# Kernel optimization log

Measured on AMD Instinct MI355X. Metric: run time of the kernel, lower is better.

## Reference

```python
import jax, jax.numpy as jnp
import numpy as np

N, E, L, S = 20000, 100000, 128, 6   # nodes, edges, latent, message-passing steps
NF, EF, TW, OUT = 11, 5, 5, 1        # node feat, edge feat, time_window, output_size
LN_EPS = 1e-5


def _mlp_ln(x, W1, b1, W2, b2, g, beta):
    # Linear -> ReLU -> Linear -> ReLU -> LayerNorm (matches torch Sequential)
    h = jax.nn.relu(x @ W1 + b1)
    h = jax.nn.relu(h @ W2 + b2)
    mu = h.mean(-1, keepdims=True)
    var = ((h - mu) ** 2).mean(-1, keepdims=True)
    return (h - mu) * jax.lax.rsqrt(var + LN_EPS) * g + beta


def setup_inputs() -> dict:
    key = jax.random.key(0)
    ks = iter(jax.random.split(key, 64))

    def w(shape):
        fan_in = shape[-2]
        return jax.random.normal(next(ks), shape, jnp.float32) / np.float32(np.sqrt(fan_in))

    inp = {
        'node_features': jax.random.normal(next(ks), (1, N, NF), jnp.float32),
        'edge_features': jax.random.normal(next(ks), (1, E, EF), jnp.float32),
        'senders': jax.random.randint(next(ks), (E,), 0, N, jnp.int32),
        'receivers': jax.random.randint(next(ks), (E,), 0, N, jnp.int32),
        'node_mean': jax.random.normal(next(ks), (NF,), jnp.float32),
        'node_std': jnp.ones((NF,), jnp.float32),
        'edge_mean': jax.random.normal(next(ks), (EF,), jnp.float32),
        'edge_std': jnp.ones((EF,), jnp.float32),
        'enc_n_W1': w((NF, L)), 'enc_n_b1': jnp.zeros((L,), jnp.float32),
        'enc_n_W2': w((L, L)), 'enc_n_b2': jnp.zeros((L,), jnp.float32),
        'enc_n_g': jnp.ones((L,), jnp.float32), 'enc_n_beta': jnp.zeros((L,), jnp.float32),
        'enc_e_W1': w((EF, L)), 'enc_e_b1': jnp.zeros((L,), jnp.float32),
        'enc_e_W2': w((L, L)), 'enc_e_b2': jnp.zeros((L,), jnp.float32),
        'enc_e_g': jnp.ones((L,), jnp.float32), 'enc_e_beta': jnp.zeros((L,), jnp.float32),
        'blk_e_W1': w((S, 3 * L, L)), 'blk_e_b1': jnp.zeros((S, L), jnp.float32),
        'blk_e_W2': w((S, L, L)), 'blk_e_b2': jnp.zeros((S, L), jnp.float32),
        'blk_e_g': jnp.ones((S, L), jnp.float32), 'blk_e_beta': jnp.zeros((S, L), jnp.float32),
        'blk_n_W1': w((S, 2 * L, L)), 'blk_n_b1': jnp.zeros((S, L), jnp.float32),
        'blk_n_W2': w((S, L, L)), 'blk_n_b2': jnp.zeros((S, L), jnp.float32),
        'blk_n_g': jnp.ones((S, L), jnp.float32), 'blk_n_beta': jnp.zeros((S, L), jnp.float32),
        'dec_W1': w((L, 8)), 'dec_b1': jnp.zeros((8,), jnp.float32),
        'dec_W2': w((8, TW)), 'dec_b2': jnp.zeros((TW,), jnp.float32),
    }
    return inp


def reference(node_features, edge_features, senders, receivers,
              node_mean, node_std, edge_mean, edge_std,
              enc_n_W1, enc_n_b1, enc_n_W2, enc_n_b2, enc_n_g, enc_n_beta,
              enc_e_W1, enc_e_b1, enc_e_W2, enc_e_b2, enc_e_g, enc_e_beta,
              blk_e_W1, blk_e_b1, blk_e_W2, blk_e_b2, blk_e_g, blk_e_beta,
              blk_n_W1, blk_n_b1, blk_n_W2, blk_n_b2, blk_n_g, blk_n_beta,
              dec_W1, dec_b1, dec_W2, dec_b2):
    # ---- encode (Normalizer in eval mode: (x - mean) / std) ----
    node_lat = _mlp_ln((node_features - node_mean) / node_std,
                       enc_n_W1, enc_n_b1, enc_n_W2, enc_n_b2, enc_n_g, enc_n_beta)  # [1,N,L]
    edge_lat = _mlp_ln((edge_features - edge_mean) / edge_std,
                       enc_e_W1, enc_e_b1, enc_e_W2, enc_e_b2, enc_e_g, enc_e_beta)  # [1,E,L]

    # ---- process: gather -> edge MLP -> scatter_add -> node MLP, residuals ----
    for i in range(S):
        e_in = jnp.concatenate([node_lat[:, senders, :], node_lat[:, receivers, :], edge_lat], axis=-1)  # [1,E,3L]
        new_e = _mlp_ln(e_in, blk_e_W1[i], blk_e_b1[i], blk_e_W2[i], blk_e_b2[i], blk_e_g[i], blk_e_beta[i])
        aggr = jax.ops.segment_sum(new_e[0], receivers, num_segments=N)[None]  # [1,N,L]
        new_n = _mlp_ln(jnp.concatenate([node_lat, aggr], axis=-1),
                        blk_n_W1[i], blk_n_b1[i], blk_n_W2[i], blk_n_b2[i], blk_n_g[i], blk_n_beta[i])
        node_lat = node_lat + new_n
        edge_lat = edge_lat + new_e

    # ---- decode: Conv1d(k=1) == per-node linear; Swish(beta=1) ----
    h = node_lat[0] @ dec_W1 + dec_b1          # [N,8]
    h = h * jax.nn.sigmoid(h)
    dec = h @ dec_W2 + dec_b2                  # [N,TW]
    dt = jnp.repeat(jnp.arange(1, TW + 1), OUT).astype(dec.dtype)  # [TW*OUT]
    delta = (dec * dt).reshape(N, TW, OUT).transpose(1, 0, 2)      # [TW,N,OUT]
    return delta
```

## Files before the change

### kernel.cpp

```cpp
#include <hip/hip_runtime.h>
#include <cstdint>
#include <cstddef>


#define N_NODES 20000
#define N_EDGES 100000
#define LDIM    128
#define NSTEPS  6

typedef float  f32x4  __attribute__((ext_vector_type(4)));
typedef __bf16 bf16x8 __attribute__((ext_vector_type(8)));

__device__ __forceinline__ bf16x8 cvt8(const float* p) {
  float4 u = *(const float4*)p;
  float4 v = *(const float4*)(p + 4);
  bf16x8 o;
  o[0] = (__bf16)u.x; o[1] = (__bf16)u.y; o[2] = (__bf16)u.z; o[3] = (__bf16)u.w;
  o[4] = (__bf16)v.x; o[5] = (__bf16)v.y; o[6] = (__bf16)v.z; o[7] = (__bf16)v.w;
  return o;
}

struct PrepArgs {
  const float *s_enW1, *s_enW2, *s_eeW1, *s_eeW2;
  const float *s_beW1, *s_beW2, *s_bnW1, *s_bnW2;
  __bf16 *d_enW1, *d_enW2, *d_eeW1, *d_eeW2;
  __bf16 *d_beW1, *d_beW2, *d_bnW1, *d_bnW2;
  int* counts;
};

__device__ __forceinline__ void swz_src(int idx, int& k, int& col) {
  int j    = idx & 7;
  int lane = (idx >> 3) & 63;
  int ct   = (idx >> 9) & 7;
  int kc   = idx >> 12;
  col = ct * 16 + (lane & 15);
  k   = kc * 32 + (lane >> 4) * 8 + j;
}

__global__ __launch_bounds__(256) void prep_kernel(PrepArgs p) {
  int idx = blockIdx.x * 256 + threadIdx.x;
  int k, col;

  if (idx < 4096) {
    swz_src(idx, k, col);
    p.d_enW1[idx] = (__bf16)((k < 11) ? p.s_enW1[k * 128 + col] : 0.f);
    return;
  }
  idx -= 4096;
  if (idx < 16384) {
    swz_src(idx, k, col);
    p.d_enW2[idx] = (__bf16)p.s_enW2[k * 128 + col];
    return;
  }
  idx -= 16384;
  if (idx < 4096) {
    swz_src(idx, k, col);
    p.d_eeW1[idx] = (__bf16)((k < 5) ? p.s_eeW1[k * 128 + col] : 0.f);
    return;
  }
  idx -= 4096;
  if (idx < 16384) {
    swz_src(idx, k, col);
    p.d_eeW2[idx] = (__bf16)p.s_eeW2[k * 128 + col];
    return;
  }
  idx -= 16384;
  if (idx < 294912) {
    int s = idx / 49152, rem = idx % 49152;
    swz_src(rem, k, col);
    p.d_beW1[idx] = (__bf16)p.s_beW1[(size_t)s * 49152 + k * 128 + col];
    return;
  }
  idx -= 294912;
  if (idx < 98304) {
    int s = idx >> 14, rem = idx & 16383;
    swz_src(rem, k, col);
    p.d_beW2[idx] = (__bf16)p.s_beW2[s * 16384 + k * 128 + col];
    return;
  }
  idx -= 98304;
  if (idx < 196608) {
    int s = idx >> 15, rem = idx & 32767;
    swz_src(rem, k, col);
    p.d_bnW1[idx] = (__bf16)p.s_bnW1[s * 32768 + k * 128 + col];
    return;
  }
  idx -= 196608;
  if (idx < 98304) {
    int s = idx >> 14, rem = idx & 16383;
    swz_src(rem, k, col);
    p.d_bnW2[idx] = (__bf16)p.s_bnW2[s * 16384 + k * 128 + col];
    return;
  }
  idx -= 98304;
  if (idx < N_NODES) p.counts[idx] = 0;
}

__global__ __launch_bounds__(256) void hist_kernel(const int* __restrict__ recv,
                                                   int* __restrict__ counts) {
  int e = blockIdx.x * 256 + threadIdx.x;
  if (e < N_EDGES) atomicAdd(&counts[recv[e]], 1);
}

__global__ __launch_bounds__(1024) void scan_kernel(const int* __restrict__ counts,
                                                    int* __restrict__ row_ptr,
                                                    int* __restrict__ cursor) {
  __shared__ int part[1024];
  const int t = threadIdx.x;
  const int base = t * 20;
  int local[20];
  int s = 0;
#pragma unroll
  for (int i = 0; i < 20; ++i) {
    int idx = base + i;
    int v = (idx < N_NODES) ? counts[idx] : 0;
    local[i] = s;
    s += v;
  }
  part[t] = s;
  __syncthreads();
  for (int off = 1; off < 1024; off <<= 1) {
    int add = (t >= off) ? part[t - off] : 0;
    __syncthreads();
    part[t] += add;
    __syncthreads();
  }
  const int excl = part[t] - s;
#pragma unroll
  for (int i = 0; i < 20; ++i) {
    int idx = base + i;
    if (idx < N_NODES) {
      int v = excl + local[i];
      row_ptr[idx] = v;
      cursor[idx]  = v;
    }
  }
  if (t == 1023) row_ptr[N_NODES] = part[1023];
}

__global__ __launch_bounds__(256) void fill_kernel(const int* __restrict__ recv,
                                                   int* __restrict__ cursor,
                                                   int* __restrict__ edge_list) {
  int e = blockIdx.x * 256 + threadIdx.x;
  if (e < N_EDGES) {
    int r = recv[e];
    int pos = atomicAdd(&cursor[r], 1);
    edge_list[pos] = e;
  }
}

struct MlpArgs {
  const float* x; const float* mean; const float* stdv;
  float* node_lat; float* edge_lat;
  __bf16* new_e;
  const int* senders; const int* receivers;
  const int* row_ptr; const int* edge_list;
  const __bf16* W1t; const __bf16* W2t;
  const float* b1; const float* b2; const float* g; const float* beta;
  int M;
};

template <int K1, int MODE>
__global__ __launch_bounds__(256, 3) void mlp2_kernel(MlpArgs a) {
  constexpr int NKC = K1 / 32;
  constexpr int RT  = 2;
  constexpr int HS  = 136;

  __shared__ __align__(16) __bf16 H1[4 * 32 * HS];

  const int tid   = threadIdx.x;
  const int lane  = tid & 63;
  const int wv    = tid >> 6;
  const int l15   = lane & 15;
  const int quad  = lane >> 4;
  const int M     = a.M;
  const int rbase = blockIdx.x * 128 + wv * 32;

  __bf16* h1w = H1 + wv * 32 * HS;

  int rowA[RT];
#pragma unroll
  for (int rt = 0; rt < RT; ++rt) {
    int r = rbase + rt * 16 + l15;
    rowA[rt] = (r < M) ? r : (M - 1);
  }

  int sA[RT], rA[RT];
  if constexpr (MODE == 2) {
#pragma unroll
    for (int rt = 0; rt < RT; ++rt) {
      sA[rt] = a.senders[rowA[rt]];
      rA[rt] = a.receivers[rowA[rt]];
    }
  }

  if constexpr (MODE == 3) {
#pragma unroll
    for (int rt = 0; rt < RT; ++rt) {
      float s[4][8];
#pragma unroll
      for (int kc = 0; kc < 4; ++kc)
#pragma unroll
        for (int j = 0; j < 8; ++j) s[kc][j] = 0.f;
      int p  = a.row_ptr[rowA[rt]];
      const int pe = a.row_ptr[rowA[rt] + 1];
      while (__any(p < pe)) {
        if (p < pe) {
          const int e = a.edge_list[p];
          const __bf16* er = a.new_e + (size_t)e * LDIM + quad * 8;
#pragma unroll
          for (int kc = 0; kc < 4; ++kc) {
            bf16x8 v = *(const bf16x8*)(er + kc * 32);
#pragma unroll
            for (int j = 0; j < 8; ++j) s[kc][j] += (float)v[j];
          }
        }
        ++p;
      }
#pragma unroll
      for (int kc = 0; kc < 4; ++kc) {
        bf16x8 o;
#pragma unroll
        for (int j = 0; j < 8; ++j) o[j] = (__bf16)s[kc][j];
        *(bf16x8*)(h1w + (rt * 16 + l15) * HS + kc * 32 + quad * 8) = o;
      }
    }
  }

  f32x4 acc[RT][8];
#pragma unroll
  for (int rt = 0; rt < RT; ++rt)
#pragma unroll
    for (int i = 0; i < 8; ++i) acc[rt][i] = (f32x4)(0.f);

#pragma unroll
  for (int kc = 0; kc < NKC; ++kc) {
    bf16x8 af[RT];
    if constexpr (MODE == 0 || MODE == 1) {
      constexpr int KIN = (MODE == 0) ? 11 : 5;
#pragma unroll
      for (int rt = 0; rt < RT; ++rt) {
        const float* xr = a.x + (size_t)rowA[rt] * KIN;
#pragma unroll
        for (int j = 0; j < 8; ++j) {
          int c = quad * 8 + j;
          float v = (c < KIN) ? (xr[c] - a.mean[c]) / a.stdv[c] : 0.f;
          af[rt][j] = (__bf16)v;
        }
      }
    } else if constexpr (MODE == 2) {
      if (kc < 4) {
#pragma unroll
        for (int rt = 0; rt < RT; ++rt)
          af[rt] = cvt8(a.node_lat + (size_t)sA[rt] * LDIM + kc * 32 + quad * 8);
      } else if (kc < 8) {
#pragma unroll
        for (int rt = 0; rt < RT; ++rt)
          af[rt] = cvt8(a.node_lat + (size_t)rA[rt] * LDIM + (kc - 4) * 32 + quad * 8);
      } else {
#pragma unroll
        for (int rt = 0; rt < RT; ++rt)
          af[rt] = cvt8(a.edge_lat + (size_t)rowA[rt] * LDIM + (kc - 8) * 32 + quad * 8);
      }
    } else {
      if (kc < 4) {
#pragma unroll
        for (int rt = 0; rt < RT; ++rt)
          af[rt] = cvt8(a.node_lat + (size_t)rowA[rt] * LDIM + kc * 32 + quad * 8);
      } else {
#pragma unroll
        for (int rt = 0; rt < RT; ++rt)
          af[rt] = *(const bf16x8*)(h1w + (rt * 16 + l15) * HS + (kc - 4) * 32 + quad * 8);
      }
    }

    bf16x8 bf[8];
#pragma unroll
    for (int ct = 0; ct < 8; ++ct)
      bf[ct] = *(const bf16x8*)(a.W1t + ((kc * 8 + ct) * 64 + lane) * 8);

#pragma unroll
    for (int rt = 0; rt < RT; ++rt)
#pragma unroll
      for (int ct = 0; ct < 8; ++ct)
        acc[rt][ct] = __builtin_amdgcn_mfma_f32_16x16x32_bf16(af[rt], bf[ct], acc[rt][ct], 0, 0, 0);
  }

#pragma unroll
  for (int ct = 0; ct < 8; ++ct) {
    const float bb = a.b1[ct * 16 + l15];
#pragma unroll
    for (int rt = 0; rt < RT; ++rt)
#pragma unroll
      for (int rr = 0; rr < 4; ++rr) {
        float v = fmaxf(acc[rt][ct][rr] + bb, 0.f);
        h1w[(rt * 16 + quad * 4 + rr) * HS + ct * 16 + l15] = (__bf16)v;
      }
  }

#pragma unroll
  for (int rt = 0; rt < RT; ++rt)
#pragma unroll
    for (int i = 0; i < 8; ++i) acc[rt][i] = (f32x4)(0.f);

#pragma unroll
  for (int kc = 0; kc < 4; ++kc) {
    bf16x8 af[RT];
#pragma unroll
    for (int rt = 0; rt < RT; ++rt)
      af[rt] = *(const bf16x8*)(h1w + (rt * 16 + l15) * HS + kc * 32 + quad * 8);
    bf16x8 bf[8];
#pragma unroll
    for (int ct = 0; ct < 8; ++ct)
      bf[ct] = *(const bf16x8*)(a.W2t + ((kc * 8 + ct) * 64 + lane) * 8);
#pragma unroll
    for (int rt = 0; rt < RT; ++rt)
#pragma unroll
      for (int ct = 0; ct < 8; ++ct)
        acc[rt][ct] = __builtin_amdgcn_mfma_f32_16x16x32_bf16(af[rt], bf[ct], acc[rt][ct], 0, 0, 0);
  }

#pragma unroll
  for (int ct = 0; ct < 8; ++ct) {
    const float bb = a.b2[ct * 16 + l15];
#pragma unroll
    for (int rt = 0; rt < RT; ++rt)
#pragma unroll
      for (int rr = 0; rr < 4; ++rr)
        acc[rt][ct][rr] = fmaxf(acc[rt][ct][rr] + bb, 0.f);
  }

  float mu[RT][4], rs[RT][4];
#pragma unroll
  for (int rt = 0; rt < RT; ++rt)
#pragma unroll
    for (int rr = 0; rr < 4; ++rr) {
      float s = 0.f, s2 = 0.f;
#pragma unroll
      for (int ct = 0; ct < 8; ++ct) { float v = acc[rt][ct][rr]; s += v; s2 += v * v; }
      s  += __shfl_xor(s, 1);  s2 += __shfl_xor(s2, 1);
      s  += __shfl_xor(s, 2);  s2 += __shfl_xor(s2, 2);
      s  += __shfl_xor(s, 4);  s2 += __shfl_xor(s2, 4);
      s  += __shfl_xor(s, 8);  s2 += __shfl_xor(s2, 8);
      float m = s * (1.f / 128.f);
      float var = fmaxf(s2 * (1.f / 128.f) - m * m, 0.f);
      mu[rt][rr] = m; rs[rt][rr] = rsqrtf(var + 1e-5f);
    }

  float gv[8], bev[8];
#pragma unroll
  for (int ct = 0; ct < 8; ++ct) {
    gv[ct]  = a.g[ct * 16 + l15];
    bev[ct] = a.beta[ct * 16 + l15];
  }

#pragma unroll
  for (int rt = 0; rt < RT; ++rt)
#pragma unroll
    for (int rr = 0; rr < 4; ++rr) {
      const int row = rbase + rt * 16 + quad * 4 + rr;
      if (row >= M) continue;
      if constexpr (MODE == 2) {
#pragma unroll
        for (int ct = 0; ct < 8; ++ct) {
          const int col = ct * 16 + l15;
          float y = (acc[rt][ct][rr] - mu[rt][rr]) * rs[rt][rr] * gv[ct] + bev[ct];
          a.edge_lat[(size_t)row * LDIM + col] += y;
          a.new_e[(size_t)row * LDIM + col] = (__bf16)y;
        }
      } else {
#pragma unroll
        for (int ct = 0; ct < 8; ++ct) {
          const int col = ct * 16 + l15;
          float y = (acc[rt][ct][rr] - mu[rt][rr]) * rs[rt][rr] * gv[ct] + bev[ct];
          if constexpr (MODE == 0)      a.node_lat[(size_t)row * LDIM + col] = y;
          else if constexpr (MODE == 1) a.edge_lat[(size_t)row * LDIM + col] = y;
          else                          a.node_lat[(size_t)row * LDIM + col] += y;
        }
      }
    }
}

__global__ __launch_bounds__(256) void decode_kernel(
    const float* __restrict__ node_lat,
    const float* __restrict__ W1, const float* __restrict__ b1,
    const float* __restrict__ W2, const float* __restrict__ b2,
    float* __restrict__ out) {
  __shared__ float X[64][129];
  const int n0 = blockIdx.x * 64;
  for (int idx = threadIdx.x; idx < 64 * 32; idx += 256) {
    int r = idx >> 5, c4 = idx & 31;
    int n = n0 + r; if (n >= N_NODES) n = N_NODES - 1;
    float4 v = *((const float4*)(node_lat + (size_t)n * 128) + c4);
    X[r][c4 * 4 + 0] = v.x; X[r][c4 * 4 + 1] = v.y;
    X[r][c4 * 4 + 2] = v.z; X[r][c4 * 4 + 3] = v.w;
  }
  __syncthreads();
  const int r = threadIdx.x;
  if (r < 64) {
    const int n = n0 + r;
    if (n < N_NODES) {
      float h[8];
#pragma unroll
      for (int j = 0; j < 8; ++j) h[j] = b1[j];
      for (int k = 0; k < 128; ++k) {
        float xv = X[r][k];
#pragma unroll
        for (int j = 0; j < 8; ++j) h[j] = fmaf(xv, W1[k * 8 + j], h[j]);
      }
#pragma unroll
      for (int j = 0; j < 8; ++j) h[j] = h[j] / (1.f + expf(-h[j]));
#pragma unroll
      for (int t = 0; t < 5; ++t) {
        float d = b2[t];
#pragma unroll
        for (int j = 0; j < 8; ++j) d = fmaf(h[j], W2[j * 5 + t], d);
        out[t * N_NODES + n] = d * (float)(t + 1);
      }
    }
  }
}

extern "C" void kernel_launch(void* const* d_in, const int* in_sizes, int n_in,
                              void* d_out, int out_size, void* d_ws, size_t ws_size,
                              hipStream_t stream) {
  (void)in_sizes; (void)n_in; (void)out_size; (void)ws_size;

  const float* node_features = (const float*)d_in[0];
  const float* edge_features = (const float*)d_in[1];
  const int*   senders       = (const int*)d_in[2];
  const int*   receivers     = (const int*)d_in[3];
  const float* node_mean = (const float*)d_in[4];
  const float* node_std  = (const float*)d_in[5];
  const float* edge_mean = (const float*)d_in[6];
  const float* edge_std  = (const float*)d_in[7];
  const float* enc_n_W1 = (const float*)d_in[8];
  const float* enc_n_b1 = (const float*)d_in[9];
  const float* enc_n_W2 = (const float*)d_in[10];
  const float* enc_n_b2 = (const float*)d_in[11];
  const float* enc_n_g    = (const float*)d_in[12];
  const float* enc_n_beta = (const float*)d_in[13];
  const float* enc_e_W1 = (const float*)d_in[14];
  const float* enc_e_b1 = (const float*)d_in[15];
  const float* enc_e_W2 = (const float*)d_in[16];
  const float* enc_e_b2 = (const float*)d_in[17];
  const float* enc_e_g    = (const float*)d_in[18];
  const float* enc_e_beta = (const float*)d_in[19];
  const float* blk_e_W1 = (const float*)d_in[20];
  const float* blk_e_b1 = (const float*)d_in[21];
  const float* blk_e_W2 = (const float*)d_in[22];
  const float* blk_e_b2 = (const float*)d_in[23];
  const float* blk_e_g    = (const float*)d_in[24];
  const float* blk_e_beta = (const float*)d_in[25];
  const float* blk_n_W1 = (const float*)d_in[26];
  const float* blk_n_b1 = (const float*)d_in[27];
  const float* blk_n_W2 = (const float*)d_in[28];
  const float* blk_n_b2 = (const float*)d_in[29];
  const float* blk_n_g    = (const float*)d_in[30];
  const float* blk_n_beta = (const float*)d_in[31];
  const float* dec_W1 = (const float*)d_in[32];
  const float* dec_b1 = (const float*)d_in[33];
  const float* dec_W2 = (const float*)d_in[34];
  const float* dec_b2 = (const float*)d_in[35];

  char* ws = (char*)d_ws;
  float*  node_lat = (float*)(ws);
  float*  edge_lat = (float*)(ws + 10240000);
  __bf16* new_e    = (__bf16*)(ws + 61440000);
  __bf16* wb       = (__bf16*)(ws + 87040000);
  int* counts    = (int*)(ws + 88498176);
  int* row_ptr   = (int*)(ws + 88578176);
  int* cursor    = (int*)(ws + 88658192);
  int* edge_list = (int*)(ws + 88738192);

  __bf16* enW1s = wb;
  __bf16* enW2s = enW1s + 4096;
  __bf16* eeW1s = enW2s + 16384;
  __bf16* eeW2s = eeW1s + 4096;
  __bf16* beW1s = eeW2s + 16384;
  __bf16* beW2s = beW1s + 6 * 49152;
  __bf16* bnW1s = beW2s + 6 * 16384;
  __bf16* bnW2s = bnW1s + 6 * 32768;

  PrepArgs pa;
  pa.s_enW1 = enc_n_W1; pa.s_enW2 = enc_n_W2; pa.s_eeW1 = enc_e_W1; pa.s_eeW2 = enc_e_W2;
  pa.s_beW1 = blk_e_W1; pa.s_beW2 = blk_e_W2; pa.s_bnW1 = blk_n_W1; pa.s_bnW2 = blk_n_W2;
  pa.d_enW1 = enW1s; pa.d_enW2 = enW2s; pa.d_eeW1 = eeW1s; pa.d_eeW2 = eeW2s;
  pa.d_beW1 = beW1s; pa.d_beW2 = beW2s; pa.d_bnW1 = bnW1s; pa.d_bnW2 = bnW2s;
  pa.counts = counts;
  prep_kernel<<<2927, 256, 0, stream>>>(pa);

  hist_kernel<<<(N_EDGES + 255) / 256, 256, 0, stream>>>(receivers, counts);
  scan_kernel<<<1, 1024, 0, stream>>>(counts, row_ptr, cursor);
  fill_kernel<<<(N_EDGES + 255) / 256, 256, 0, stream>>>(receivers, cursor, edge_list);

  const int NODE_BLOCKS = (N_NODES + 127) / 128;
  const int EDGE_BLOCKS = (N_EDGES + 127) / 128;
  const int DEC_BLOCKS  = (N_NODES + 63) / 64;

  MlpArgs base;
  base.node_lat = node_lat; base.edge_lat = edge_lat; base.new_e = new_e;
  base.senders = senders; base.receivers = receivers;
  base.row_ptr = row_ptr; base.edge_list = edge_list;
  base.x = nullptr; base.mean = nullptr; base.stdv = nullptr;

  {
    MlpArgs a = base;
    a.x = node_features; a.mean = node_mean; a.stdv = node_std;
    a.W1t = enW1s; a.W2t = enW2s;
    a.b1 = enc_n_b1; a.b2 = enc_n_b2; a.g = enc_n_g; a.beta = enc_n_beta;
    a.M = N_NODES;
    mlp2_kernel<32, 0><<<NODE_BLOCKS, 256, 0, stream>>>(a);
  }
  {
    MlpArgs a = base;
    a.x = edge_features; a.mean = edge_mean; a.stdv = edge_std;
    a.W1t = eeW1s; a.W2t = eeW2s;
    a.b1 = enc_e_b1; a.b2 = enc_e_b2; a.g = enc_e_g; a.beta = enc_e_beta;
    a.M = N_EDGES;
    mlp2_kernel<32, 1><<<EDGE_BLOCKS, 256, 0, stream>>>(a);
  }

  for (int i = 0; i < NSTEPS; ++i) {
    {
      MlpArgs a = base;
      a.W1t = beW1s + (size_t)i * 49152; a.W2t = beW2s + (size_t)i * 16384;
      a.b1 = blk_e_b1 + i * 128; a.b2 = blk_e_b2 + i * 128;
      a.g = blk_e_g + i * 128; a.beta = blk_e_beta + i * 128;
      a.M = N_EDGES;
      mlp2_kernel<384, 2><<<EDGE_BLOCKS, 256, 0, stream>>>(a);
    }
    {
      MlpArgs a = base;
      a.W1t = bnW1s + (size_t)i * 32768; a.W2t = bnW2s + (size_t)i * 16384;
      a.b1 = blk_n_b1 + i * 128; a.b2 = blk_n_b2 + i * 128;
      a.g = blk_n_g + i * 128; a.beta = blk_n_beta + i * 128;
      a.M = N_NODES;
      mlp2_kernel<256, 3><<<NODE_BLOCKS, 256, 0, stream>>>(a);
    }
  }

  decode_kernel<<<DEC_BLOCKS, 256, 0, stream>>>(
      node_lat, dec_W1, dec_b1, dec_W2, dec_b2, (float*)d_out);
}
```

Baseline: 818.5 us.

## Move segment-sum aggregation into a dedicated wave-per-node kernel

Moves the per-node sum of incoming edge messages out of the node MLP kernel into a separate agg_kernel. There, one wavefront handles one node: edge ids are loaded cooperatively and broadcast by shuffle, and each lane sums two bf16 columns. The node MLP then reads the aggregate from a global bf16 buffer. This removes the divergent, degree-imbalanced per-row loop inside the MFMA kernel, which could stall whole tiles. The cost is an extra kernel launch per step and an extra global write and read of an N×128 bf16 buffer.

```diff
diff --git a/kernel.cpp b/kernel.cpp
--- a/kernel.cpp
+++ b/kernel.cpp
@@ -10,6 +10,7 @@
 
 typedef float  f32x4  __attribute__((ext_vector_type(4)));
 typedef __bf16 bf16x8 __attribute__((ext_vector_type(8)));
+typedef __bf16 bf16x2 __attribute__((ext_vector_type(2)));
 
 __device__ __forceinline__ bf16x8 cvt8(const float* p) {
   float4 u = *(const float4*)p;
@@ -149,12 +150,38 @@
   }
 }
 
+__global__ __launch_bounds__(256) void agg_kernel(
+    const int* __restrict__ row_ptr, const int* __restrict__ edge_list,
+    const __bf16* __restrict__ new_e, __bf16* __restrict__ aggr_bf) {
+  const int wv   = threadIdx.x >> 6;
+  const int lane = threadIdx.x & 63;
+  const int n    = blockIdx.x * 4 + wv;
+  if (n >= N_NODES) return;
+  int p = row_ptr[n];
+  const int pe = row_ptr[n + 1];
+  float s0 = 0.f, s1 = 0.f;
+  while (p < pe) {
+    const int cnt = min(pe - p, 64);
+    int eid = (lane < cnt) ? edge_list[p + lane] : 0;
+    for (int j = 0; j < cnt; ++j) {
+      const int e = __shfl(eid, j);
+      bf16x2 v = *(const bf16x2*)(new_e + (size_t)e * LDIM + lane * 2);
+      s0 += (float)v[0];
+      s1 += (float)v[1];
+    }
+    p += cnt;
+  }
+  bf16x2 o;
+  o[0] = (__bf16)s0; o[1] = (__bf16)s1;
+  *(bf16x2*)(aggr_bf + (size_t)n * LDIM + lane * 2) = o;
+}
+
 struct MlpArgs {
   const float* x; const float* mean; const float* stdv;
   float* node_lat; float* edge_lat;
   __bf16* new_e;
+  const __bf16* aggr_bf;
   const int* senders; const int* receivers;
-  const int* row_ptr; const int* edge_list;
   const __bf16* W1t; const __bf16* W2t;
   const float* b1; const float* b2; const float* g; const float* beta;
   int M;
@@ -194,39 +221,6 @@
     }
   }
 
-  if constexpr (MODE == 3) {
-#pragma unroll
-    for (int rt = 0; rt < RT; ++rt) {
-      float s[4][8];
-#pragma unroll
-      for (int kc = 0; kc < 4; ++kc)
-#pragma unroll
-        for (int j = 0; j < 8; ++j) s[kc][j] = 0.f;
-      int p  = a.row_ptr[rowA[rt]];
-      const int pe = a.row_ptr[rowA[rt] + 1];
-      while (__any(p < pe)) {
-        if (p < pe) {
-          const int e = a.edge_list[p];
-          const __bf16* er = a.new_e + (size_t)e * LDIM + quad * 8;
-#pragma unroll
-          for (int kc = 0; kc < 4; ++kc) {
-            bf16x8 v = *(const bf16x8*)(er + kc * 32);
-#pragma unroll
-            for (int j = 0; j < 8; ++j) s[kc][j] += (float)v[j];
-          }
-        }
-        ++p;
-      }
-#pragma unroll
-      for (int kc = 0; kc < 4; ++kc) {
-        bf16x8 o;
-#pragma unroll
-        for (int j = 0; j < 8; ++j) o[j] = (__bf16)s[kc][j];
-        *(bf16x8*)(h1w + (rt * 16 + l15) * HS + kc * 32 + quad * 8) = o;
-      }
-    }
-  }
-
   f32x4 acc[RT][8];
 #pragma unroll
   for (int rt = 0; rt < RT; ++rt)
@@ -270,7 +264,7 @@
       } else {
 #pragma unroll
         for (int rt = 0; rt < RT; ++rt)
-          af[rt] = *(const bf16x8*)(h1w + (rt * 16 + l15) * HS + (kc - 4) * 32 + quad * 8);
+          af[rt] = *(const bf16x8*)(a.aggr_bf + (size_t)rowA[rt] * LDIM + (kc - 4) * 32 + quad * 8);
       }
     }
 
@@ -472,6 +466,7 @@
   int* row_ptr   = (int*)(ws + 88578176);
   int* cursor    = (int*)(ws + 88658192);
   int* edge_list = (int*)(ws + 88738192);
+  __bf16* aggr_bf = (__bf16*)(ws + 89138192);
 
   __bf16* enW1s = wb;
   __bf16* enW2s = enW1s + 4096;
@@ -497,11 +492,12 @@
   const int NODE_BLOCKS = (N_NODES + 127) / 128;
   const int EDGE_BLOCKS = (N_EDGES + 127) / 128;
   const int DEC_BLOCKS  = (N_NODES + 63) / 64;
+  const int AGG_BLOCKS  = (N_NODES + 3) / 4;
 
   MlpArgs base;
   base.node_lat = node_lat; base.edge_lat = edge_lat; base.new_e = new_e;
+  base.aggr_bf = aggr_bf;
   base.senders = senders; base.receivers = receivers;
-  base.row_ptr = row_ptr; base.edge_list = edge_list;
   base.x = nullptr; base.mean = nullptr; base.stdv = nullptr;
 
   {
@@ -530,6 +526,7 @@
       a.M = N_EDGES;
       mlp2_kernel<384, 2><<<EDGE_BLOCKS, 256, 0, stream>>>(a);
     }
+    agg_kernel<<<AGG_BLOCKS, 256, 0, stream>>>(row_ptr, edge_list, new_e, aggr_bf);
     {
       MlpArgs a = base;
       a.W1t = bnW1s + (size_t)i * 32768; a.W2t = bnW2s + (size_t)i * 16384;
```

New measurement: 782.2 us. -4.4%, faster.
